# Kernel optimization log

Measured on AMD Instinct MI355X. Metric: run time of the kernel, lower is better.

## Reference

```python
import jax, jax.numpy as jnp
import numpy as np

OVERSAMP = 2.0
D = 2  # spatial dims


def _pad_center(x, grid):
    # centered zero-pad of last D dims from im_size to grid (PadLast)
    H, W = x.shape[-2], x.shape[-1]
    ph, pw = grid[0] - H, grid[1] - W
    pads = [(0, 0)] * (x.ndim - 2) + [(ph // 2, ph - ph // 2), (pw // 2, pw - pw // 2)]
    return jnp.pad(x, pads)


def _crop_center(x, im_size):
    # adjoint of centered pad: crop last D dims back to im_size
    H2, W2 = x.shape[-2], x.shape[-1]
    ph, pw = H2 - im_size[0], W2 - im_size[1]
    return x[..., ph // 2: ph // 2 + im_size[0], pw // 2: pw // 2 + im_size[1]]


def setup_inputs() -> dict:
    key = jax.random.key(0)
    ks = jax.random.split(key, 6)
    N, A, C, H, W = 2, 5, 12, 256, 256
    G = (2 * H, 2 * W)  # oversampled grid for toeplitz kernels
    return {
        "x_r": jax.random.normal(ks[0], (N, A, H, W), jnp.float32),
        "x_i": jax.random.normal(ks[1], (N, A, H, W), jnp.float32),
        "mps_r": jax.random.normal(ks[2], (C, H, W), jnp.float32) * 0.3,
        "mps_i": jax.random.normal(ks[3], (C, H, W), jnp.float32) * 0.3,
        "kernels_r": jax.random.normal(ks[4], (A, A) + G, jnp.float32) * 0.1,
        "kernels_i": jax.random.normal(ks[5], (A, A) + G, jnp.float32) * 0.1,
    }


def reference(x_r, x_i, mps_r, mps_i, kernels_r, kernels_i):
    # Toeplitz normal operator AHA_func from SubspaceLinopFactory.get_normal_toeplitz,
    # fully vectorized over coils (C) and subspace coefficients (A).
    x = x_r + 1j * x_i                    # [N, A, H, W]
    mps = mps_r + 1j * mps_i              # [C, H, W]
    kernels = kernels_r + 1j * kernels_i  # [A_out, A_in, 2H, 2W]
    im_size = x.shape[-2:]
    grid = kernels.shape[-2:]
    axes = (-2, -1)

    # x.unsqueeze(coildim) * mps[:, None]  -> [N, C, A, H, W]
    xm = x[:, None, :, :, :] * mps[None, :, None, :, :]
    # PadLast: centered zero-pad to the oversampled grid
    xp = _pad_center(xm, grid)                             # [N, C, A, 2H, 2W]
    Fx = jnp.fft.fftn(xp, axes=axes, norm="ortho")         # [N, C, A_in, 2H, 2W]
    # Fx.unsqueeze(2) * kernels[A_out, A_in], summed over A_in
    G = jnp.einsum("ncahw,bahw->ncbhw", Fx, kernels)       # [N, C, A_out, 2H, 2W]
    y = (OVERSAMP ** D) * jnp.fft.ifftn(G, axes=axes, norm="ortho")
    yc = _crop_center(y, im_size)                          # [N, C, A_out, H, W]
    # multiply conj coil maps, sum over coils
    out = jnp.einsum("ncahw,chw->nahw", yc, jnp.conj(mps))  # [N, A, H, W] complex64
    return out
```

## Files before the change

### kernel.cpp

```cpp
#include <hip/hip_runtime.h>
#include <math.h>

#define N_ 2
#define A_ 5
#define C_ 12
#define H_ 256
#define G_ 512
#define SCALE_ (4.0f / 262144.0f)
#define OUTF_ 655360
#define HALFF_ 327680
#define IMGC_ 131072
#define NCG_ 4

struct __attribute__((aligned(4))) h2 { _Float16 x, y; };
struct __attribute__((aligned(8))) h2x2 { _Float16 x0, y0, x1, y1; };
__device__ __forceinline__ float2 ld2(const h2* p, size_t i) {
    h2 v = p[i]; return make_float2((float)v.x, (float)v.y);
}
__device__ __forceinline__ void st2(h2* p, size_t i, float2 v) {
    float x = fminf(fmaxf(v.x, -60000.f), 60000.f);
    float y = fminf(fmaxf(v.y, -60000.f), 60000.f);
    h2 o; o.x = (_Float16)x; o.y = (_Float16)y; p[i] = o;
}

__device__ __forceinline__ float2 cmul(float2 a, float2 b) {
    return make_float2(a.x * b.x - a.y * b.y, a.x * b.y + a.y * b.x);
}

__device__ __forceinline__ float4 qadd(float4 a, float4 b) {
    return make_float4(a.x + b.x, a.y + b.y, a.z + b.z, a.w + b.w);
}
__device__ __forceinline__ float4 qsub(float4 a, float4 b) {
    return make_float4(a.x - b.x, a.y - b.y, a.z - b.z, a.w - b.w);
}
__device__ __forceinline__ float4 qmul(float4 a, float4 w) {
    return make_float4(a.x * w.x - a.y * w.y, a.x * w.y + a.y * w.x,
                       a.z * w.z - a.w * w.w, a.z * w.w + a.w * w.z);
}
__device__ __forceinline__ float4 qmulc(float4 a, float4 w) {
    return make_float4(a.x * w.x + a.y * w.y, a.y * w.x - a.x * w.y,
                       a.z * w.z + a.w * w.w, a.w * w.z - a.z * w.w);
}
__device__ __forceinline__ int PHI(int i) { return i ^ ((i >> 3) & 7); }

__device__ __forceinline__ void build_twS(float2* twS, int t) {
    if (t < 256) {
        float s, c;
        sincosf(-6.283185307179586f * (float)t * (1.0f / 512.0f), &s, &c);
        twS[t] = make_float2(c, s);
    }
    __syncthreads();
    int off = 256;
    #pragma unroll
    for (int sh = 1; sh <= 8; sh++) {
        int sz = 256 >> sh;
        if (t < sz) twS[off + t] = twS[t << sh];
        off += sz;
    }
    __syncthreads();
}

__device__ __forceinline__ void fwd_quad(float4* D, const float4* tw4,
                                         int bt, int M4, int offA4) {
    int jf = bt & (M4 - 1);
    int f0 = ((bt & ~(M4 - 1)) << 2) | jf;
    float4 x0 = D[PHI(f0)],          x1 = D[PHI(f0 + M4)];
    float4 x2 = D[PHI(f0 + 2 * M4)], x3 = D[PHI(f0 + 3 * M4)];
    float4 tA  = tw4[offA4 + jf];
    float4 tA2 = tw4[offA4 + M4 + jf];
    float4 tB  = tw4[offA4 + 2 * M4 + jf];
    float4 u0 = qadd(x0, x2), v0 = qmul(qsub(x0, x2), tA);
    float4 u1 = qadd(x1, x3), v1 = qmul(qsub(x1, x3), tA2);
    D[PHI(f0)]          = qadd(u0, u1);
    D[PHI(f0 + M4)]     = qmul(qsub(u0, u1), tB);
    D[PHI(f0 + 2 * M4)] = qadd(v0, v1);
    D[PHI(f0 + 3 * M4)] = qmul(qsub(v0, v1), tB);
}
__device__ __forceinline__ void fwd_quad0(float4* D, const float4* tw4, int bt) {
    int f0 = bt;
    float4 x1 = D[PHI(f0 + 64)];
    float4 x2 = D[PHI(f0 + 128)];
    float4 tA  = tw4[f0];
    float4 tA2 = tw4[64 + f0];
    float4 tB  = tw4[128 + f0];
    float4 zero = make_float4(0.f, 0.f, 0.f, 0.f);
    float4 v0 = qmul(qsub(zero, x2), tA);
    float4 v1 = qmul(x1, tA2);
    D[PHI(f0)]       = qadd(x2, x1);
    D[PHI(f0 + 64)]  = qmul(qsub(x2, x1), tB);
    D[PHI(f0 + 128)] = qadd(v0, v1);
    D[PHI(f0 + 192)] = qmul(qsub(v0, v1), tB);
}
__device__ __forceinline__ void inv_quad(float4* D, const float4* tw4,
                                         int bt, int M2, int offM4, int off2M4) {
    int jf = bt & (M2 - 1);
    int f0 = ((bt & ~(M2 - 1)) << 2) | jf;
    float4 x0 = D[PHI(f0)],          x1 = D[PHI(f0 + M2)];
    float4 x2 = D[PHI(f0 + 2 * M2)], x3 = D[PHI(f0 + 3 * M2)];
    float4 wA  = tw4[offM4 + jf];
    float4 wB0 = tw4[off2M4 + jf];
    float4 wB1 = tw4[off2M4 + M2 + jf];
    float4 t1 = qmulc(x1, wA), t3 = qmulc(x3, wA);
    float4 u0 = qadd(x0, t1), u1 = qsub(x0, t1);
    float4 u2 = qadd(x2, t3), u3 = qsub(x2, t3);
    float4 s2 = qmulc(u2, wB0), s3 = qmulc(u3, wB1);
    D[PHI(f0)]          = qadd(u0, s2);
    D[PHI(f0 + M2)]     = qadd(u1, s3);
    D[PHI(f0 + 2 * M2)] = qsub(u0, s2);
    D[PHI(f0 + 3 * M2)] = qsub(u1, s3);
}
__device__ __forceinline__ void inv_quad_crop(float4* D, const float4* tw4,
                                              int bt) {
    int f0 = bt;
    float4 x0 = D[PHI(f0)],       x1 = D[PHI(f0 + 64)];
    float4 x2 = D[PHI(f0 + 128)], x3 = D[PHI(f0 + 192)];
    float4 wA  = tw4[128 + f0];
    float4 wB0 = tw4[f0];
    float4 wB1 = tw4[64 + f0];
    float4 t1 = qmulc(x1, wA), t3 = qmulc(x3, wA);
    float4 u0 = qadd(x0, t1), u1 = qsub(x0, t1);
    float4 u2 = qadd(x2, t3), u3 = qsub(x2, t3);
    float4 s2 = qmulc(u2, wB0), s3 = qmulc(u3, wB1);
    D[PHI(f0 + 64)]  = qadd(u1, s3);
    D[PHI(f0 + 128)] = qsub(u0, s2);
}

__device__ void fft512_dif(float2* d, const float2* twS, int t) {
    int off = 0;
    #pragma unroll
    for (int m = 256; m >= 1; m >>= 1) {
        if (m >= 64) __syncthreads();
        else __builtin_amdgcn_wave_barrier();
        int j = t & (m - 1);
        int p = ((t & ~(m - 1)) << 1) | j;
        int q = p + m;
        float2 a = d[p], b = d[q];
        d[p] = make_float2(a.x + b.x, a.y + b.y);
        float2 s = make_float2(a.x - b.x, a.y - b.y);
        d[q] = cmul(s, twS[off + j]);
        off += m;
    }
    __syncthreads();
}
__device__ void ifft512_dit(float2* d, const float2* twS, int t) {
    int off = 510;
    #pragma unroll
    for (int m = 1; m <= 256; m <<= 1) {
        if (m == 1 || m >= 128) __syncthreads();
        else __builtin_amdgcn_wave_barrier();
        int j = t & (m - 1);
        int p = ((t & ~(m - 1)) << 1) | j;
        int q = p + m;
        float2 w = twS[off + j];
        w.y = -w.y;
        float2 b = cmul(d[q], w);
        float2 a = d[p];
        d[p] = make_float2(a.x + b.x, a.y + b.y);
        d[q] = make_float2(a.x - b.x, a.y - b.y);
        off -= (m << 1);
    }
    __syncthreads();
}


__device__ __forceinline__ void r_body(int blk, const float* __restrict__ kr,
                                       const float* __restrict__ ki, h2* Krev,
                                       int t) {
    int p = blk >> 9;
    int h = blk & 511;
    size_t base = ((size_t)p * G_ + h) * G_;
    int j0 = __brev((unsigned)t) >> 23;
    int j1 = __brev((unsigned)(t + 256)) >> 23;
    st2(Krev, base + t,       make_float2(kr[base + j0], ki[base + j0]));
    st2(Krev, base + t + 256, make_float2(kr[base + j1], ki[base + j1]));
}

__device__ __forceinline__ void a2_body(int blk,
    const float* __restrict__ xr, const float* __restrict__ xi,
    const float* __restrict__ mr, const float* __restrict__ mi,
    h2* P, int n0, int t, float2* twS, float4 (*rows4)[262]) {
    int oct = blk & 31;
    int rest = blk >> 5;
    int c  = rest % 12;
    int nl = rest / 12;
    int n  = n0 + nl;
    build_twS(twS, t);
    const float4* tw4 = (const float4*)twS;

    int r = t & 7;
    int wc = oct * 8 + r;
    float mR[8], mI[8];
    #pragma unroll
    for (int k = 0; k < 8; k++) {
        int h = (t >> 3) + 32 * k;
        size_t mo = ((size_t)c * H_ + h) * H_ + wc;
        mR[k] = mr[mo]; mI[k] = mi[mo];
    }
    float2* rowf2 = (float2*)&rows4[r][0];
    int wv = t >> 6, ln = t & 63;
    float4* d0 = &rows4[2 * wv][0];
    float4* d1 = &rows4[2 * wv + 1][0];

    for (int a = 0; a < 5; a++) {
        #pragma unroll
        for (int k = 0; k < 8; k++) {
            int h = (t >> 3) + 32 * k;
            size_t xo = (((size_t)n * A_ + a) * H_ + h) * H_ + wc;
            float xr_ = xr[xo], xi_ = xi[xo];
            int e = h + 128;
            rowf2[2 * PHI(e >> 1) + (e & 1)] =
                make_float2(xr_ * mR[k] - xi_ * mI[k],
                            xr_ * mI[k] + xi_ * mR[k]);
        }
        __syncthreads();

        fwd_quad0(d0, tw4, ln);         fwd_quad0(d1, tw4, ln);
        __builtin_amdgcn_wave_barrier();
        fwd_quad(d0, tw4, ln, 16, 192); fwd_quad(d1, tw4, ln, 16, 192);
        __builtin_amdgcn_wave_barrier();
        fwd_quad(d0, tw4, ln, 4, 240);  fwd_quad(d1, tw4, ln, 4, 240);
        __builtin_amdgcn_wave_barrier();
        fwd_quad(d0, tw4, ln, 1, 252);  fwd_quad(d1, tw4, ln, 1, 252);
        __syncthreads();

        h2* Pp = P + (size_t)((nl * 12 + c) * 5 + a) * IMGC_;
        #pragma unroll
        for (int k = 0; k < 16; k++) {
            int jh = k * 32 + (t >> 3);
            float4 v = rows4[r][PHI(jh >> 1)];
            float2 res = (jh & 1) ? make_float2(v.x - v.z, v.y - v.w)
                                  : make_float2(v.x + v.z, v.y + v.w);
            st2(Pp, (size_t)jh * 256 + oct * 8 + r, res);
        }
        __syncthreads();
    }
}

#define NA2_ (2 * C_ * 32)
#define NR_  (25 * 512)
#define NZ_  (OUTF_ / 256)

__global__ __launch_bounds__(256)
void kernelU(const float* __restrict__ xr, const float* __restrict__ xi,
             const float* __restrict__ mr, const float* __restrict__ mi,
             const float* __restrict__ kr, const float* __restrict__ ki,
             h2* P, h2* Krev, float* outf) {
    __shared__ float2 twS[512];
    __shared__ float4 rows4[8][262];
    int blk = blockIdx.x;
    int t = threadIdx.x;
    if (blk < NA2_) {
        a2_body(blk, xr, xi, mr, mi, P, 0, t, twS, rows4);
    } else if (blk < NA2_ + NR_) {
        r_body(blk - NA2_, kr, ki, Krev, t);
    } else {
        outf[(size_t)(blk - NA2_ - NR_) * 256 + t] = 0.f;
    }
}

__global__ __launch_bounds__(256)
void zeroF(float* outf, int base) {
    outf[(size_t)base + blockIdx.x * 256 + threadIdx.x] = 0.f;
}

__global__ __launch_bounds__(256)
void kernelR(const float* __restrict__ kr, const float* __restrict__ ki,
             h2* Krev) {
    r_body(blockIdx.x, kr, ki, Krev, threadIdx.x);
}

__global__ __launch_bounds__(256)
void kernelA2(const float* __restrict__ xr, const float* __restrict__ xi,
              const float* __restrict__ mr, const float* __restrict__ mi,
              h2* P, int n0, int nspan) {
    (void)nspan;
    __shared__ float2 twS[512];
    __shared__ float4 rows4[8][262];
    a2_body(blockIdx.x, xr, xi, mr, mi, P, n0, threadIdx.x, twS, rows4);
}

__global__ __launch_bounds__(320)
void kernelB2(const h2* __restrict__ Krev, h2* P, int nspan) {
    int blk = blockIdx.x;
    int xcd = blk & 7;
    int idx = blk >> 3;
    int cn  = 12 * nspan;
    int jh  = xcd * 64 + idx / cn;
    int rem = idx % cn;
    int c   = rem % 12;
    int nl  = rem / 12;
    int htrue = __brev((unsigned)jh) >> 23;
    int t = threadIdx.x;
    __shared__ float2 twS[512];
    __shared__ float4 Fa4[5][256];
    build_twS(twS, t);
    const float4* tw4 = (const float4*)twS;
    int wv = t >> 6, ln = t & 63;
    size_t pbase = (size_t)((nl * 12 + c) * 5) * IMGC_ + (size_t)jh * 256;

    float2* Ff2 = (float2*)&Fa4[wv][0];
    const h2* Pa = P + pbase + (size_t)wv * IMGC_;
    #pragma unroll
    for (int k = 0; k < 4; k++) {
        int e = ln + 64 * k;
        float2 v = ld2(Pa, e);
        int ec = e + 128;
        Ff2[2 * PHI(ec >> 1) + (ec & 1)] = v;
    }
    __builtin_amdgcn_wave_barrier();

    float4* D = &Fa4[wv][0];
    fwd_quad0(D, tw4, ln);         __builtin_amdgcn_wave_barrier();
    fwd_quad(D, tw4, ln, 16, 192); __builtin_amdgcn_wave_barrier();
    fwd_quad(D, tw4, ln, 4, 240);  __builtin_amdgcn_wave_barrier();
    fwd_quad(D, tw4, ln, 1, 252);
    __syncthreads();

    if (t < 256) {
        float2 f0[5], f1[5];
        #pragma unroll
        for (int a = 0; a < 5; a++) {
            float4 x = Fa4[a][PHI(t)];
            f0[a] = make_float2(x.x + x.z, x.y + x.w);
            f1[a] = make_float2(x.x - x.z, x.y - x.w);
        }
        const h2x2* Kp = reinterpret_cast<const h2x2*>(Krev);
        #pragma unroll
        for (int b = 0; b < 5; b++) {
            float2 a0 = make_float2(0.f, 0.f);
            float2 a1 = make_float2(0.f, 0.f);
            #pragma unroll
            for (int a = 0; a < 5; a++) {
                h2x2 kv = Kp[((size_t)(b * 5 + a) * G_ + htrue) * 256 + t];
                float k0x = (float)kv.x0, k0y = (float)kv.y0;
                float k1x = (float)kv.x1, k1y = (float)kv.y1;
                a0.x += k0x * f0[a].x - k0y * f0[a].y;
                a0.y += k0x * f0[a].y + k0y * f0[a].x;
                a1.x += k1x * f1[a].x - k1y * f1[a].y;
                a1.y += k1x * f1[a].y + k1y * f1[a].x;
            }
            Fa4[b][PHI(t)] =
                make_float4(a0.x + a1.x, a0.y + a1.y, a0.x - a1.x, a0.y - a1.y);
        }
    }
    __syncthreads();

    inv_quad(D, tw4, ln, 1, 254, 252);  __builtin_amdgcn_wave_barrier();
    inv_quad(D, tw4, ln, 4, 248, 240);  __builtin_amdgcn_wave_barrier();
    inv_quad(D, tw4, ln, 16, 224, 192); __builtin_amdgcn_wave_barrier();
    inv_quad_crop(D, tw4, ln);
    __builtin_amdgcn_wave_barrier();

    h2* Pb = P + pbase + (size_t)wv * IMGC_;
    #pragma unroll
    for (int k = 0; k < 4; k++) {
        int e = ln + 64 * k;
        int ec = e + 128;
        float2 v = Ff2[2 * PHI(ec >> 1) + (ec & 1)];
        st2(Pb, e, v);
    }
}

__global__ __launch_bounds__(256)
void kernelC2(const float* __restrict__ mr, const float* __restrict__ mi,
              const h2* __restrict__ P, float* outf, int n0, int nspan) {
    int blk = blockIdx.x;
    int oct = blk & 31;
    int b   = (blk >> 5) % 5;
    int rest = blk / 160;
    int cg = rest % NCG_;
    int nl = rest / NCG_;
    int n  = n0 + nl;
    int t = threadIdx.x;
    __shared__ float2 twS[512];
    __shared__ float4 rows4[8][262];
    build_twS(twS, t);
    const float4* tw4 = (const float4*)twS;

    int r = t & 7;
    int wc = oct * 8 + r;
    int wv = t >> 6, ln = t & 63;
    float4* d0 = &rows4[2 * wv][0];
    float4* d1 = &rows4[2 * wv + 1][0];
    const float2* rowf2 = (const float2*)&rows4[r][0];

    float acc[8];
    #pragma unroll
    for (int k = 0; k < 8; k++) acc[k] = 0.f;

    for (int ci = 0; ci < 3; ci++) {
        int c = cg * 3 + ci;
        const h2* Pb = P + (size_t)((nl * 12 + c) * 5 + b) * IMGC_;
        #pragma unroll
        for (int k = 0; k < 8; k++) {
            int jh0 = k * 64 + (t >> 3) * 2;
            float2 p0 = ld2(Pb, (size_t)jh0 * 256 + wc);
            float2 p1 = ld2(Pb, (size_t)(jh0 + 1) * 256 + wc);
            rows4[r][PHI(jh0 >> 1)] =
                make_float4(p0.x + p1.x, p0.y + p1.y, p0.x - p1.x, p0.y - p1.y);
        }
        __syncthreads();

        inv_quad(d0, tw4, ln, 1, 254, 252);  inv_quad(d1, tw4, ln, 1, 254, 252);
        __builtin_amdgcn_wave_barrier();
        inv_quad(d0, tw4, ln, 4, 248, 240);  inv_quad(d1, tw4, ln, 4, 248, 240);
        __builtin_amdgcn_wave_barrier();
        inv_quad(d0, tw4, ln, 16, 224, 192); inv_quad(d1, tw4, ln, 16, 224, 192);
        __builtin_amdgcn_wave_barrier();
        inv_quad_crop(d0, tw4, ln);          inv_quad_crop(d1, tw4, ln);
        __syncthreads();

        #pragma unroll
        for (int k = 0; k < 8; k++) {
            int hh = (t >> 3) + 32 * k;
            int e = hh + 128;
            float2 v = rowf2[2 * PHI(e >> 1) + (e & 1)];
            size_t mo = (((size_t)c) * H_ + hh) * H_ + wc;
            acc[k] += mr[mo] * v.x + mi[mo] * v.y;
        }
        __syncthreads();
    }

    #pragma unroll
    for (int k = 0; k < 8; k++) {
        int hh = (t >> 3) + 32 * k;
        size_t idx = (((size_t)n * A_ + b) * H_ + hh) * H_ + wc;
        unsafeAtomicAdd(&outf[idx], acc[k] * SCALE_);
    }
}


__global__ __launch_bounds__(256)
void kernelA(const float* __restrict__ xr, const float* __restrict__ xi,
             const float* __restrict__ mr, const float* __restrict__ mi,
             h2* X1, int n, int c, int a) {
    int oct = blockIdx.x;
    int t = threadIdx.x;
    __shared__ float2 twS[512];
    __shared__ float2 rows[8][516];
    build_twS(twS, t);

    int r = t & 7;
    int wc = oct * 8 + r;
    #pragma unroll
    for (int k = 0; k < 8; k++) {
        int h = (t >> 3) + 32 * k;
        size_t xo = (((size_t)n * A_ + a) * H_ + h) * H_ + wc;
        size_t mo = (((size_t)c) * H_ + h) * H_ + wc;
        float xr_ = xr[xo], xi_ = xi[xo];
        float mr_ = mr[mo], mi_ = mi[mo];
        rows[r][h + 128] = make_float2(xr_ * mr_ - xi_ * mi_,
                                       xr_ * mi_ + xi_ * mr_);
        rows[r][(h < 128) ? h : (h + 256)] = make_float2(0.f, 0.f);
    }
    __syncthreads();
    for (int rr = 0; rr < 8; rr++) fft512_dif(&rows[rr][0], twS, t);

    #pragma unroll
    for (int k = 0; k < 16; k++) {
        int jh = k * 32 + (t >> 3);
        st2(X1, (size_t)jh * 256 + oct * 8 + (t & 7), rows[t & 7][jh]);
    }
}

__global__ __launch_bounds__(256)
void kernelB(const float* __restrict__ kr, const float* __restrict__ ki,
             const h2* X1, h2* X2, int b, int a) {
    int jh = blockIdx.x;
    int htrue = __brev((unsigned)jh) >> 23;
    int t = threadIdx.x;
    __shared__ float2 twS[512];
    __shared__ float2 F[512];
    __shared__ float2 g[512];
    build_twS(twS, t);

    float2 v = ld2(X1, (size_t)jh * 256 + t);
    F[t + 128] = v;
    F[(t < 128) ? t : (t + 256)] = make_float2(0.f, 0.f);
    __syncthreads();
    fft512_dif(F, twS, t);

    #pragma unroll
    for (int half = 0; half < 2; half++) {
        int jw = t + half * 256;
        int wtrue = __brev((unsigned)jw) >> 23;
        size_t kidx = (((size_t)(b * A_ + a)) * G_ + htrue) * G_ + wtrue;
        g[jw] = cmul(make_float2(kr[kidx], ki[kidx]), F[jw]);
    }
    ifft512_dit(g, twS, t);

    float2 res = g[t + 128];
    size_t o = (size_t)jh * 256 + t;
    if (a == 0) st2(X2, o, res);
    else {
        float2 cur = ld2(X2, o);
        st2(X2, o, make_float2(cur.x + res.x, cur.y + res.y));
    }
}

__global__ __launch_bounds__(256)
void kernelC(const float* __restrict__ mr, const float* __restrict__ mi,
             const h2* X2, float* outf, int n, int c, int b) {
    int oct = blockIdx.x;
    int t = threadIdx.x;
    __shared__ float2 twS[512];
    __shared__ float2 rows[8][516];
    build_twS(twS, t);

    #pragma unroll
    for (int k = 0; k < 16; k++) {
        int jh = k * 32 + (t >> 3);
        rows[t & 7][jh] = ld2(X2, (size_t)jh * 256 + oct * 8 + (t & 7));
    }
    for (int rr = 0; rr < 8; rr++) ifft512_dit(&rows[rr][0], twS, t);

    int r = t & 7;
    int wc = oct * 8 + r;
    #pragma unroll
    for (int k = 0; k < 8; k++) {
        int hh = (t >> 3) + 32 * k;
        float2 v = rows[r][hh + 128];
        size_t mo = (((size_t)c) * H_ + hh) * H_ + wc;
        float m_r = mr[mo], m_i = mi[mo];
        float re = (m_r * v.x + m_i * v.y) * SCALE_;
        size_t idx = (((size_t)n * A_ + b) * H_ + hh) * H_ + wc;
        outf[idx] += re;
    }
}

extern "C" void kernel_launch(void* const* d_in, const int* in_sizes, int n_in,
                              void* d_out, int out_size, void* d_ws, size_t ws_size,
                              hipStream_t stream) {
    const float* xr = (const float*)d_in[0];
    const float* xi = (const float*)d_in[1];
    const float* mr = (const float*)d_in[2];
    const float* mi = (const float*)d_in[3];
    const float* kr = (const float*)d_in[4];
    const float* ki = (const float*)d_in[5];
    float* outf = (float*)d_out;
    (void)in_sizes; (void)n_in; (void)out_size;

    const size_t KREV_BYTES = 25ull * G_ * G_ * sizeof(h2);
    const size_t PLANES1    = 60ull * IMGC_ * sizeof(h2);
    const size_t PLANES2    = 120ull * IMGC_ * sizeof(h2);

    if (d_ws != nullptr && ws_size >= PLANES2 + KREV_BYTES) {
        h2* P    = (h2*)d_ws;
        h2* Krev = (h2*)((char*)d_ws + PLANES2);
        kernelU<<<NA2_ + NR_ + NZ_, 256, 0, stream>>>(xr, xi, mr, mi, kr, ki,
                                                      P, Krev, outf);
        kernelB2<<<2 * C_ * 512, 320, 0, stream>>>(Krev, P, 2);
        kernelC2<<<2 * A_ * 32 * NCG_, 256, 0, stream>>>(mr, mi, P, outf, 0, 2);
        return;
    }

    if (d_ws != nullptr && ws_size >= PLANES1 + KREV_BYTES) {
        h2* P    = (h2*)d_ws;
        h2* Krev = (h2*)((char*)d_ws + PLANES1);
        zeroF<<<OUTF_ / 256, 256, 0, stream>>>(outf, 0);
        kernelR<<<25 * 512, 256, 0, stream>>>(kr, ki, Krev);
        for (int n = 0; n < N_; n++) {
            kernelA2<<<C_ * 32, 256, 0, stream>>>(xr, xi, mr, mi, P, n, 1);
            kernelB2<<<C_ * 512, 320, 0, stream>>>(Krev, P, 1);
            kernelC2<<<A_ * 32 * NCG_, 256, 0, stream>>>(mr, mi, P, outf, n, 1);
        }
        return;
    }

    zeroF<<<HALFF_ / 256, 256, 0, stream>>>(outf, 0);
    {
        h2* X1 = (h2*)(outf + HALFF_);
        h2* X2 = (h2*)(outf + HALFF_ + IMGC_);
        for (int c = 0; c < C_; c++)
            for (int b = 0; b < A_; b++) {
                for (int a = 0; a < A_; a++) {
                    kernelA<<<32, 256, 0, stream>>>(xr, xi, mr, mi, X1, 0, c, a);
                    kernelB<<<512, 256, 0, stream>>>(kr, ki, X1, X2, b, a);
                }
                kernelC<<<32, 256, 0, stream>>>(mr, mi, X2, outf, 0, c, b);
            }
    }

    zeroF<<<HALFF_ / 256, 256, 0, stream>>>(outf, HALFF_);
    {
        h2* X1 = (h2*)d_in[0];
        h2* X2 = (h2*)d_in[1];
        for (int c = 0; c < C_; c++)
            for (int b = 0; b < A_; b++) {
                for (int a = 0; a < A_; a++) {
                    kernelA<<<32, 256, 0, stream>>>(xr, xi, mr, mi, X1, 1, c, a);
                    kernelB<<<512, 256, 0, stream>>>(kr, ki, X1, X2, b, a);
                }
                kernelC<<<32, 256, 0, stream>>>(mr, mi, X2, outf, 1, c, b);
            }
    }
}
```

Baseline: 388.3 us.

## Split A2 blocks per subspace coefficient and pack two rows per B2 block

The first-stage FFT kernel now launches one block per (n, c, a, column-octet) instead of looping over the five coefficients inside a block. This gives five times more blocks for better GPU fill, at the cost of reloading coil maps and rebuilding twiddles in each block. The B2 kernel now processes two frequency rows per 640-thread block with doubled shared memory, halving the block count and amortizing twiddle setup. Larger blocks with more LDS may reduce occupancy.

```diff
diff --git a/kernel.cpp b/kernel.cpp
--- a/kernel.cpp
+++ b/kernel.cpp
@@ -180,7 +180,8 @@
     const float* __restrict__ mr, const float* __restrict__ mi,
     h2* P, int n0, int t, float2* twS, float4 (*rows4)[262]) {
     int oct = blk & 31;
-    int rest = blk >> 5;
+    int a   = (blk >> 5) % 5;
+    int rest = blk / 160;
     int c  = rest % 12;
     int nl = rest / 12;
     int n  = n0 + nl;
@@ -189,54 +190,44 @@
 
     int r = t & 7;
     int wc = oct * 8 + r;
-    float mR[8], mI[8];
+    float2* rowf2 = (float2*)&rows4[r][0];
     #pragma unroll
     for (int k = 0; k < 8; k++) {
         int h = (t >> 3) + 32 * k;
-        size_t mo = ((size_t)c * H_ + h) * H_ + wc;
-        mR[k] = mr[mo]; mI[k] = mi[mo];
-    }
-    float2* rowf2 = (float2*)&rows4[r][0];
+        size_t xo = (((size_t)n * A_ + a) * H_ + h) * H_ + wc;
+        size_t mo = (((size_t)c) * H_ + h) * H_ + wc;
+        float xr_ = xr[xo], xi_ = xi[xo];
+        float mr_ = mr[mo], mi_ = mi[mo];
+        int e = h + 128;
+        rowf2[2 * PHI(e >> 1) + (e & 1)] =
+            make_float2(xr_ * mr_ - xi_ * mi_, xr_ * mi_ + xi_ * mr_);
+    }
+    __syncthreads();
+
     int wv = t >> 6, ln = t & 63;
     float4* d0 = &rows4[2 * wv][0];
     float4* d1 = &rows4[2 * wv + 1][0];
-
-    for (int a = 0; a < 5; a++) {
-        #pragma unroll
-        for (int k = 0; k < 8; k++) {
-            int h = (t >> 3) + 32 * k;
-            size_t xo = (((size_t)n * A_ + a) * H_ + h) * H_ + wc;
-            float xr_ = xr[xo], xi_ = xi[xo];
-            int e = h + 128;
-            rowf2[2 * PHI(e >> 1) + (e & 1)] =
-                make_float2(xr_ * mR[k] - xi_ * mI[k],
-                            xr_ * mI[k] + xi_ * mR[k]);
-        }
-        __syncthreads();
-
-        fwd_quad0(d0, tw4, ln);         fwd_quad0(d1, tw4, ln);
-        __builtin_amdgcn_wave_barrier();
-        fwd_quad(d0, tw4, ln, 16, 192); fwd_quad(d1, tw4, ln, 16, 192);
-        __builtin_amdgcn_wave_barrier();
-        fwd_quad(d0, tw4, ln, 4, 240);  fwd_quad(d1, tw4, ln, 4, 240);
-        __builtin_amdgcn_wave_barrier();
-        fwd_quad(d0, tw4, ln, 1, 252);  fwd_quad(d1, tw4, ln, 1, 252);
-        __syncthreads();
-
-        h2* Pp = P + (size_t)((nl * 12 + c) * 5 + a) * IMGC_;
-        #pragma unroll
-        for (int k = 0; k < 16; k++) {
-            int jh = k * 32 + (t >> 3);
-            float4 v = rows4[r][PHI(jh >> 1)];
-            float2 res = (jh & 1) ? make_float2(v.x - v.z, v.y - v.w)
-                                  : make_float2(v.x + v.z, v.y + v.w);
-            st2(Pp, (size_t)jh * 256 + oct * 8 + r, res);
-        }
-        __syncthreads();
-    }
-}
-
-#define NA2_ (2 * C_ * 32)
+    fwd_quad0(d0, tw4, ln);         fwd_quad0(d1, tw4, ln);
+    __builtin_amdgcn_wave_barrier();
+    fwd_quad(d0, tw4, ln, 16, 192); fwd_quad(d1, tw4, ln, 16, 192);
+    __builtin_amdgcn_wave_barrier();
+    fwd_quad(d0, tw4, ln, 4, 240);  fwd_quad(d1, tw4, ln, 4, 240);
+    __builtin_amdgcn_wave_barrier();
+    fwd_quad(d0, tw4, ln, 1, 252);  fwd_quad(d1, tw4, ln, 1, 252);
+    __syncthreads();
+
+    h2* Pp = P + (size_t)((nl * 12 + c) * 5 + a) * IMGC_;
+    #pragma unroll
+    for (int k = 0; k < 16; k++) {
+        int jh = k * 32 + (t >> 3);
+        float4 v = rows4[r][PHI(jh >> 1)];
+        float2 res = (jh & 1) ? make_float2(v.x - v.z, v.y - v.w)
+                              : make_float2(v.x + v.z, v.y + v.w);
+        st2(Pp, (size_t)jh * 256 + oct * 8 + r, res);
+    }
+}
+
+#define NA2_ (2 * C_ * A_ * 32)
 #define NR_  (25 * 512)
 #define NZ_  (OUTF_ / 256)
 
@@ -279,26 +270,29 @@
     a2_body(blockIdx.x, xr, xi, mr, mi, P, n0, threadIdx.x, twS, rows4);
 }
 
-__global__ __launch_bounds__(320)
+__global__ __launch_bounds__(640)
 void kernelB2(const h2* __restrict__ Krev, h2* P, int nspan) {
     int blk = blockIdx.x;
     int xcd = blk & 7;
     int idx = blk >> 3;
     int cn  = 12 * nspan;
-    int jh  = xcd * 64 + idx / cn;
-    int rem = idx % cn;
+    int pair = idx / cn;
+    int rem  = idx % cn;
     int c   = rem % 12;
     int nl  = rem / 12;
+    int t = threadIdx.x;
+    int g  = t / 320;
+    int tl = t - g * 320;
+    int jh = xcd * 64 + pair * 2 + g;
     int htrue = __brev((unsigned)jh) >> 23;
-    int t = threadIdx.x;
-    __shared__ float2 twS[512];
-    __shared__ float4 Fa4[5][256];
+    __shared__ float2 twS[512];
+    __shared__ float4 Fa4[2][5][256];
     build_twS(twS, t);
     const float4* tw4 = (const float4*)twS;
-    int wv = t >> 6, ln = t & 63;
+    int wv = tl >> 6, ln = tl & 63;
     size_t pbase = (size_t)((nl * 12 + c) * 5) * IMGC_ + (size_t)jh * 256;
 
-    float2* Ff2 = (float2*)&Fa4[wv][0];
+    float2* Ff2 = (float2*)&Fa4[g][wv][0];
     const h2* Pa = P + pbase + (size_t)wv * IMGC_;
     #pragma unroll
     for (int k = 0; k < 4; k++) {
@@ -309,18 +303,18 @@
     }
     __builtin_amdgcn_wave_barrier();
 
-    float4* D = &Fa4[wv][0];
+    float4* D = &Fa4[g][wv][0];
     fwd_quad0(D, tw4, ln);         __builtin_amdgcn_wave_barrier();
     fwd_quad(D, tw4, ln, 16, 192); __builtin_amdgcn_wave_barrier();
     fwd_quad(D, tw4, ln, 4, 240);  __builtin_amdgcn_wave_barrier();
     fwd_quad(D, tw4, ln, 1, 252);
     __syncthreads();
 
-    if (t < 256) {
+    if (tl < 256) {
         float2 f0[5], f1[5];
         #pragma unroll
         for (int a = 0; a < 5; a++) {
-            float4 x = Fa4[a][PHI(t)];
+            float4 x = Fa4[g][a][PHI(tl)];
             f0[a] = make_float2(x.x + x.z, x.y + x.w);
             f1[a] = make_float2(x.x - x.z, x.y - x.w);
         }
@@ -331,7 +325,7 @@
             float2 a1 = make_float2(0.f, 0.f);
             #pragma unroll
             for (int a = 0; a < 5; a++) {
-                h2x2 kv = Kp[((size_t)(b * 5 + a) * G_ + htrue) * 256 + t];
+                h2x2 kv = Kp[((size_t)(b * 5 + a) * G_ + htrue) * 256 + tl];
                 float k0x = (float)kv.x0, k0y = (float)kv.y0;
                 float k1x = (float)kv.x1, k1y = (float)kv.y1;
                 a0.x += k0x * f0[a].x - k0y * f0[a].y;
@@ -339,7 +333,7 @@
                 a1.x += k1x * f1[a].x - k1y * f1[a].y;
                 a1.y += k1x * f1[a].y + k1y * f1[a].x;
             }
-            Fa4[b][PHI(t)] =
+            Fa4[g][b][PHI(tl)] =
                 make_float4(a0.x + a1.x, a0.y + a1.y, a0.x - a1.x, a0.y - a1.y);
         }
     }
@@ -549,7 +543,7 @@
         h2* Krev = (h2*)((char*)d_ws + PLANES2);
         kernelU<<<NA2_ + NR_ + NZ_, 256, 0, stream>>>(xr, xi, mr, mi, kr, ki,
                                                       P, Krev, outf);
-        kernelB2<<<2 * C_ * 512, 320, 0, stream>>>(Krev, P, 2);
+        kernelB2<<<8 * 32 * 12 * 2, 640, 0, stream>>>(Krev, P, 2);
         kernelC2<<<2 * A_ * 32 * NCG_, 256, 0, stream>>>(mr, mi, P, outf, 0, 2);
         return;
     }
@@ -560,8 +554,8 @@
         zeroF<<<OUTF_ / 256, 256, 0, stream>>>(outf, 0);
         kernelR<<<25 * 512, 256, 0, stream>>>(kr, ki, Krev);
         for (int n = 0; n < N_; n++) {
-            kernelA2<<<C_ * 32, 256, 0, stream>>>(xr, xi, mr, mi, P, n, 1);
-            kernelB2<<<C_ * 512, 320, 0, stream>>>(Krev, P, 1);
+            kernelA2<<<C_ * A_ * 32, 256, 0, stream>>>(xr, xi, mr, mi, P, n, 1);
+            kernelB2<<<8 * 32 * 12, 640, 0, stream>>>(Krev, P, 1);
             kernelC2<<<A_ * 32 * NCG_, 256, 0, stream>>>(mr, mi, P, outf, n, 1);
         }
         return;
```

New measurement: 426.4 us. 9.8% more time.
